# Kernel tuning notes

Hardware: AMD Instinct MI355X
Metric: run time of the kernel (lower is better)

Reference implementation:

```python
import math
import jax, jax.numpy as jnp
import numpy as np

HEADS = 16
MASKED_BIAS = -10000.0


def setup_inputs() -> dict:
    key = jax.random.key(0)
    kq, kk, kv = jax.random.split(key, 3)
    B, S, D = 4, 1024, 2048
    q = jax.random.normal(kq, (B, S, D), dtype=jnp.float32)
    k = jax.random.normal(kk, (B, S, D), dtype=jnp.float32)
    v = jax.random.normal(kv, (B, S, D), dtype=jnp.float32)
    return {"q": q, "k": k, "v": v}


def _mha(q, k, v):
    B, Sq, D = q.shape
    Sk = k.shape[-2]
    hd = D // HEADS
    # (B, H, S, hd)
    qh = q.reshape(B, Sq, HEADS, hd).transpose(0, 2, 1, 3)
    kh = k.reshape(B, Sk, HEADS, hd).transpose(0, 2, 1, 3)
    vh = v.reshape(B, Sk, HEADS, hd).transpose(0, 2, 1, 3)
    scores = jnp.einsum("bhqd,bhkd->bhqk", qh, kh) / math.sqrt(hd)
    # causal mask: query i attends to keys <= i (aligned to end of kv)
    qi = jnp.arange(Sq)[:, None] + (Sk - Sq)
    ki = jnp.arange(Sk)[None, :]
    causal = ki <= qi  # (Sq, Sk)
    scores = jnp.where(causal[None, None], scores, jnp.asarray(MASKED_BIAS, scores.dtype))
    attn = jax.nn.softmax(scores, axis=-1)
    out = jnp.einsum("bhqk,bhkd->bhqd", attn, vh)
    return out.transpose(0, 2, 1, 3).reshape(B, Sq, D)


def reference(q, k, v):
    return _mha(q, k, v)
```

## Files before the change

### kernel.cpp

```cpp
#include <hip/hip_runtime.h>
#include <hip/hip_bf16.h>


#define HEADS  16
#define HD     128
#define SEQ    1024
#define DMODEL 2048

typedef _Float16 f16;
typedef __attribute__((ext_vector_type(8))) _Float16 f16x8;
typedef __attribute__((ext_vector_type(4))) _Float16 f16x4;
typedef __attribute__((ext_vector_type(4))) float    f32x4;
typedef __attribute__((ext_vector_type(4))) unsigned int u32x4;

__device__ __forceinline__ unsigned int pkrtz(float a, float b) {
    return __builtin_bit_cast(unsigned int, __builtin_amdgcn_cvt_pkrtz(a, b));
}

__global__ __launch_bounds__(256, 2)
void fa_fwd(const float* __restrict__ Q,
            const float* __restrict__ K,
            const float* __restrict__ V,
            float* __restrict__ O)
{
    __shared__ f16 kT[64 * 128];
    __shared__ f16 vT[128 * 64];

    const int tid  = threadIdx.x;
    const int lane = tid & 63;
    const int wv   = tid >> 6;
    const int quad = lane >> 4;
    const int cl   = lane & 15;

    const int bh = blockIdx.x;
    const int qt = 15 - blockIdx.y;
    const int qb = qt * 64;
    const long long head_off = ((long long)(bh >> 4) * SEQ) * DMODEL
                             + (long long)(bh & 15) * HD;
    const float rscale = 0.08838834764831845f;

    const int krow = tid >> 4;
    const int kg   = tid & 15;
    const int kgs  = kg ^ krow;
    const int vr0  = (tid & 31) * 2;
    const int vcg  = tid >> 5;
    const int vg   = vr0 >> 3;
    const int vo   = vr0 & 7;

    f32x4 kraw[8], vraw[8];

    auto loadKV = [&](int kbase) {
        #pragma unroll
        for (int i = 0; i < 4; ++i) {
            const float* kp = K + head_off + (long long)(kbase + krow + i * 16) * DMODEL + kg * 8;
            kraw[2 * i]     = *(const f32x4*)kp;
            kraw[2 * i + 1] = *(const f32x4*)(kp + 4);
        }
        const float* vp = V + head_off + (long long)(kbase + vr0) * DMODEL + vcg * 16;
        #pragma unroll
        for (int j = 0; j < 4; ++j) {
            vraw[j]     = *(const f32x4*)(vp + 4 * j);
            vraw[4 + j] = *(const f32x4*)(vp + DMODEL + 4 * j);
        }
    };

    const int qrow = qb + wv * 16 + cl;
    f16x8 qf[4];
    {
        const float* qp = Q + head_off + (long long)qrow * DMODEL + quad * 8;
        #pragma unroll
        for (int kk = 0; kk < 4; ++kk) {
            f32x4 qa = *(const f32x4*)(qp + kk * 32);
            f32x4 qc = *(const f32x4*)(qp + kk * 32 + 4);
            union { f16x8 v; unsigned int u[4]; } qw;
            qw.u[0] = pkrtz(qa[0], qa[1]);
            qw.u[1] = pkrtz(qa[2], qa[3]);
            qw.u[2] = pkrtz(qc[0], qc[1]);
            qw.u[3] = pkrtz(qc[2], qc[3]);
            qf[kk] = qw.v;
        }
    }

    f32x4 acc[8];
    #pragma unroll
    for (int i = 0; i < 8; ++i) acc[i] = (f32x4){0.f, 0.f, 0.f, 0.f};
    float ls = 0.f;

    loadKV(0);

    #pragma unroll 1
    for (int kt = 0; kt <= qt; ++kt) {
        __syncthreads();

        #pragma unroll
        for (int i = 0; i < 4; ++i) {
            u32x4 w;
            w.x = pkrtz(kraw[2 * i][0], kraw[2 * i][1]);
            w.y = pkrtz(kraw[2 * i][2], kraw[2 * i][3]);
            w.z = pkrtz(kraw[2 * i + 1][0], kraw[2 * i + 1][1]);
            w.w = pkrtz(kraw[2 * i + 1][2], kraw[2 * i + 1][3]);
            *(u32x4*)&kT[(krow + 16 * i) * 128 + kgs * 8] = w;
        }
        #pragma unroll
        for (int j = 0; j < 16; ++j) {
            unsigned int pk = pkrtz(vraw[j >> 2][j & 3], vraw[4 + (j >> 2)][j & 3]);
            *(unsigned int*)&vT[(vcg * 16 + j) * 64 + ((vg ^ (j & 7)) * 8) + vo] = pk;
        }
        __syncthreads();

        if (kt < qt) loadKV((kt + 1) * 64);

        f32x4 sc[4];
        #pragma unroll
        for (int st = 0; st < 4; ++st) sc[st] = (f32x4){0.f, 0.f, 0.f, 0.f};
        #pragma unroll
        for (int kk = 0; kk < 4; ++kk) {
            #pragma unroll
            for (int st = 0; st < 4; ++st) {
                f16x8 kf = *(const f16x8*)&kT[(st * 16 + cl) * 128
                                              + ((kk * 4 + quad) ^ cl) * 8];
                sc[st] = __builtin_amdgcn_mfma_f32_16x16x32_f16(kf, qf[kk], sc[st], 0, 0, 0);
            }
        }

        const int kbase = kt * 64;
        f16x4 pf[4];
        if (kt == qt) {
            #pragma unroll
            for (int st = 0; st < 4; ++st) {
                float e[4];
                #pragma unroll
                for (int r = 0; r < 4; ++r) {
                    int key = kbase + st * 16 + quad * 4 + r;
                    float ex = __expf(sc[st][r] * rscale);
                    e[r] = (key <= qrow) ? ex : 0.f;
                    ls += e[r];
                }
                union { f16x4 v; unsigned int u[2]; } pw;
                pw.u[0] = pkrtz(e[0], e[1]);
                pw.u[1] = pkrtz(e[2], e[3]);
                pf[st] = pw.v;
            }
        } else {
            #pragma unroll
            for (int st = 0; st < 4; ++st) {
                float e[4];
                #pragma unroll
                for (int r = 0; r < 4; ++r) {
                    e[r] = __expf(sc[st][r] * rscale);
                    ls += e[r];
                }
                union { f16x4 v; unsigned int u[2]; } pw;
                pw.u[0] = pkrtz(e[0], e[1]);
                pw.u[1] = pkrtz(e[2], e[3]);
                pf[st] = pw.v;
            }
        }

        #pragma unroll
        for (int dt = 0; dt < 8; ++dt) {
            #pragma unroll
            for (int st = 0; st < 4; ++st) {
                f16x4 vf = *(const f16x4*)&vT[(dt * 16 + cl) * 64
                                              + ((st * 2 + (quad >> 1)) ^ (cl & 7)) * 8
                                              + (quad & 1) * 4];
                acc[dt] = __builtin_amdgcn_mfma_f32_16x16x16f16(vf, pf[st], acc[dt], 0, 0, 0);
            }
        }
    }

    float lsum = ls;
    lsum += __shfl_xor(lsum, 16, 64);
    lsum += __shfl_xor(lsum, 32, 64);
    const float rl = 1.0f / lsum;

    float* op = O + head_off + (long long)qrow * DMODEL + quad * 4;
    #pragma unroll
    for (int dt = 0; dt < 8; ++dt) {
        f32x4 o4 = acc[dt];
        o4[0] *= rl; o4[1] *= rl; o4[2] *= rl; o4[3] *= rl;
        *(f32x4*)(op + dt * 16) = o4;
    }
}

extern "C" void kernel_launch(void* const* d_in, const int* in_sizes, int n_in,
                              void* d_out, int out_size, void* d_ws, size_t ws_size,
                              hipStream_t stream) {
    const float* q = (const float*)d_in[0];
    const float* k = (const float*)d_in[1];
    const float* v = (const float*)d_in[2];
    float* o = (float*)d_out;

    dim3 grid(4 * HEADS, SEQ / 64);
    dim3 block(256);
    fa_fwd<<<grid, block, 0, stream>>>(q, k, v, o);
}
```

Before: 169.2 us.

## Process two 64-row query tiles per block to reuse each K/V tile

```diff
diff --git a/kernel.cpp b/kernel.cpp
--- a/kernel.cpp
+++ b/kernel.cpp
@@ -33,8 +33,9 @@
     const int cl   = lane & 15;
 
     const int bh = blockIdx.x;
-    const int qt = 15 - blockIdx.y;
-    const int qb = qt * 64;
+    const int yy = blockIdx.y;
+    const int qt = (yy < 4) ? (7 - yy) : (yy - 4);
+    const int qb = qt * 128;
     const long long head_off = ((long long)(bh >> 4) * SEQ) * DMODEL
                              + (long long)(bh & 15) * HD;
     const float rscale = 0.08838834764831845f;
@@ -64,10 +65,12 @@
         }
     };
 
-    const int qrow = qb + wv * 16 + cl;
-    f16x8 qf[4];
-    {
-        const float* qp = Q + head_off + (long long)qrow * DMODEL + quad * 8;
+    const int qrow0 = qb + wv * 16 + cl;
+    const int qrow1 = qrow0 + 64;
+    f16x8 qf[2][4];
+    #pragma unroll
+    for (int g = 0; g < 2; ++g) {
+        const float* qp = Q + head_off + (long long)(g ? qrow1 : qrow0) * DMODEL + quad * 8;
         #pragma unroll
         for (int kk = 0; kk < 4; ++kk) {
             f32x4 qa = *(const f32x4*)(qp + kk * 32);
@@ -77,19 +80,23 @@
             qw.u[1] = pkrtz(qa[2], qa[3]);
             qw.u[2] = pkrtz(qc[0], qc[1]);
             qw.u[3] = pkrtz(qc[2], qc[3]);
-            qf[kk] = qw.v;
-        }
-    }
-
-    f32x4 acc[8];
+            qf[g][kk] = qw.v;
+        }
+    }
+
+    f32x4 acc[8][2];
     #pragma unroll
-    for (int i = 0; i < 8; ++i) acc[i] = (f32x4){0.f, 0.f, 0.f, 0.f};
-    float ls = 0.f;
+    for (int i = 0; i < 8; ++i) {
+        acc[i][0] = (f32x4){0.f, 0.f, 0.f, 0.f};
+        acc[i][1] = (f32x4){0.f, 0.f, 0.f, 0.f};
+    }
+    float ls0 = 0.f, ls1 = 0.f;
 
     loadKV(0);
+    const int last = 2 * qt + 1;
 
     #pragma unroll 1
-    for (int kt = 0; kt <= qt; ++kt) {
+    for (int kt = 0; kt <= last; ++kt) {
         __syncthreads();
 
         #pragma unroll
@@ -108,78 +115,133 @@
         }
         __syncthreads();
 
-        if (kt < qt) loadKV((kt + 1) * 64);
-
-        f32x4 sc[4];
-        #pragma unroll
-        for (int st = 0; st < 4; ++st) sc[st] = (f32x4){0.f, 0.f, 0.f, 0.f};
-        #pragma unroll
-        for (int kk = 0; kk < 4; ++kk) {
+        if (kt < last) loadKV((kt + 1) * 64);
+
+        const int kbase = kt * 64;
+        f16x4 pf[4][2];
+
+        if (kt <= 2 * qt) {
+            f32x4 sc[4][2];
             #pragma unroll
             for (int st = 0; st < 4; ++st) {
-                f16x8 kf = *(const f16x8*)&kT[(st * 16 + cl) * 128
-                                              + ((kk * 4 + quad) ^ cl) * 8];
-                sc[st] = __builtin_amdgcn_mfma_f32_16x16x32_f16(kf, qf[kk], sc[st], 0, 0, 0);
-            }
-        }
-
-        const int kbase = kt * 64;
-        f16x4 pf[4];
-        if (kt == qt) {
+                sc[st][0] = (f32x4){0.f, 0.f, 0.f, 0.f};
+                sc[st][1] = (f32x4){0.f, 0.f, 0.f, 0.f};
+            }
+            #pragma unroll
+            for (int kk = 0; kk < 4; ++kk) {
+                #pragma unroll
+                for (int st = 0; st < 4; ++st) {
+                    f16x8 kf = *(const f16x8*)&kT[(st * 16 + cl) * 128
+                                                  + ((kk * 4 + quad) ^ cl) * 8];
+                    sc[st][0] = __builtin_amdgcn_mfma_f32_16x16x32_f16(kf, qf[0][kk], sc[st][0], 0, 0, 0);
+                    sc[st][1] = __builtin_amdgcn_mfma_f32_16x16x32_f16(kf, qf[1][kk], sc[st][1], 0, 0, 0);
+                }
+            }
+
+            if (kt == 2 * qt) {
+                #pragma unroll
+                for (int st = 0; st < 4; ++st) {
+                    float e0[4], e1[4];
+                    #pragma unroll
+                    for (int r = 0; r < 4; ++r) {
+                        const int key = kbase + st * 16 + quad * 4 + r;
+                        float ex = __expf(sc[st][0][r] * rscale);
+                        e0[r] = (key <= qrow0) ? ex : 0.f;
+                        e1[r] = __expf(sc[st][1][r] * rscale);
+                        ls0 += e0[r]; ls1 += e1[r];
+                    }
+                    union { f16x4 v; unsigned int u[2]; } p0, p1;
+                    p0.u[0] = pkrtz(e0[0], e0[1]); p0.u[1] = pkrtz(e0[2], e0[3]);
+                    p1.u[0] = pkrtz(e1[0], e1[1]); p1.u[1] = pkrtz(e1[2], e1[3]);
+                    pf[st][0] = p0.v; pf[st][1] = p1.v;
+                }
+            } else {
+                #pragma unroll
+                for (int st = 0; st < 4; ++st) {
+                    float e0[4], e1[4];
+                    #pragma unroll
+                    for (int r = 0; r < 4; ++r) {
+                        e0[r] = __expf(sc[st][0][r] * rscale);
+                        e1[r] = __expf(sc[st][1][r] * rscale);
+                        ls0 += e0[r]; ls1 += e1[r];
+                    }
+                    union { f16x4 v; unsigned int u[2]; } p0, p1;
+                    p0.u[0] = pkrtz(e0[0], e0[1]); p0.u[1] = pkrtz(e0[2], e0[3]);
+                    p1.u[0] = pkrtz(e1[0], e1[1]); p1.u[1] = pkrtz(e1[2], e1[3]);
+                    pf[st][0] = p0.v; pf[st][1] = p1.v;
+                }
+            }
+
+            #pragma unroll
+            for (int dt = 0; dt < 8; ++dt) {
+                #pragma unroll
+                for (int st = 0; st < 4; ++st) {
+                    f16x4 vf = *(const f16x4*)&vT[(dt * 16 + cl) * 64
+                                                  + ((st * 2 + (quad >> 1)) ^ (cl & 7)) * 8
+                                                  + (quad & 1) * 4];
+                    acc[dt][0] = __builtin_amdgcn_mfma_f32_16x16x16f16(vf, pf[st][0], acc[dt][0], 0, 0, 0);
+                    acc[dt][1] = __builtin_amdgcn_mfma_f32_16x16x16f16(vf, pf[st][1], acc[dt][1], 0, 0, 0);
+                }
+            }
+        } else {
+            f32x4 sc1[4];
+            #pragma unroll
+            for (int st = 0; st < 4; ++st) sc1[st] = (f32x4){0.f, 0.f, 0.f, 0.f};
+            #pragma unroll
+            for (int kk = 0; kk < 4; ++kk) {
+                #pragma unroll
+                for (int st = 0; st < 4; ++st) {
+                    f16x8 kf = *(const f16x8*)&kT[(st * 16 + cl) * 128
+                                                  + ((kk * 4 + quad) ^ cl) * 8];
+                    sc1[st] = __builtin_amdgcn_mfma_f32_16x16x32_f16(kf, qf[1][kk], sc1[st], 0, 0, 0);
+                }
+            }
             #pragma unroll
             for (int st = 0; st < 4; ++st) {
-                float e[4];
+                float e1[4];
                 #pragma unroll
                 for (int r = 0; r < 4; ++r) {
-                    int key = kbase + st * 16 + quad * 4 + r;
-                    float ex = __expf(sc[st][r] * rscale);
-                    e[r] = (key <= qrow) ? ex : 0.f;
-                    ls += e[r];
-                }
-                union { f16x4 v; unsigned int u[2]; } pw;
-                pw.u[0] = pkrtz(e[0], e[1]);
-                pw.u[1] = pkrtz(e[2], e[3]);
-                pf[st] = pw.v;
-            }
-        } else {
-            #pragma unroll
-            for (int st = 0; st < 4; ++st) {
-                float e[4];
-                #pragma unroll
-                for (int r = 0; r < 4; ++r) {
-                    e[r] = __expf(sc[st][r] * rscale);
-                    ls += e[r];
-                }
-                union { f16x4 v; unsigned int u[2]; } pw;
-                pw.u[0] = pkrtz(e[0], e[1]);
-                pw.u[1] = pkrtz(e[2], e[3]);
-                pf[st] = pw.v;
-            }
-        }
-
-        #pragma unroll
-        for (int dt = 0; dt < 8; ++dt) {
-            #pragma unroll
-            for (int st = 0; st < 4; ++st) {
-                f16x4 vf = *(const f16x4*)&vT[(dt * 16 + cl) * 64
-                                              + ((st * 2 + (quad >> 1)) ^ (cl & 7)) * 8
-                                              + (quad & 1) * 4];
-                acc[dt] = __builtin_amdgcn_mfma_f32_16x16x16f16(vf, pf[st], acc[dt], 0, 0, 0);
-            }
-        }
-    }
-
-    float lsum = ls;
-    lsum += __shfl_xor(lsum, 16, 64);
-    lsum += __shfl_xor(lsum, 32, 64);
-    const float rl = 1.0f / lsum;
-
-    float* op = O + head_off + (long long)qrow * DMODEL + quad * 4;
+                    const int key = kbase + st * 16 + quad * 4 + r;
+                    float ex = __expf(sc1[st][r] * rscale);
+                    e1[r] = (key <= qrow1) ? ex : 0.f;
+                    ls1 += e1[r];
+                }
+                union { f16x4 v; unsigned int u[2]; } p1;
+                p1.u[0] = pkrtz(e1[0], e1[1]); p1.u[1] = pkrtz(e1[2], e1[3]);
+                pf[st][1] = p1.v;
+            }
+            #pragma unroll
+            for (int dt = 0; dt < 8; ++dt) {
+                #pragma unroll
+                for (int st = 0; st < 4; ++st) {
+                    f16x4 vf = *(const f16x4*)&vT[(dt * 16 + cl) * 64
+                                                  + ((st * 2 + (quad >> 1)) ^ (cl & 7)) * 8
+                                                  + (quad & 1) * 4];
+                    acc[dt][1] = __builtin_amdgcn_mfma_f32_16x16x16f16(vf, pf[st][1], acc[dt][1], 0, 0, 0);
+                }
+            }
+        }
+    }
+
+    float l0 = ls0;
+    l0 += __shfl_xor(l0, 16, 64);
+    l0 += __shfl_xor(l0, 32, 64);
+    float l1 = ls1;
+    l1 += __shfl_xor(l1, 16, 64);
+    l1 += __shfl_xor(l1, 32, 64);
+    const float rl0 = 1.0f / l0;
+    const float rl1 = 1.0f / l1;
+
+    float* op0 = O + head_off + (long long)qrow0 * DMODEL + quad * 4;
+    float* op1 = O + head_off + (long long)qrow1 * DMODEL + quad * 4;
     #pragma unroll
     for (int dt = 0; dt < 8; ++dt) {
-        f32x4 o4 = acc[dt];
-        o4[0] *= rl; o4[1] *= rl; o4[2] *= rl; o4[3] *= rl;
-        *(f32x4*)(op + dt * 16) = o4;
+        f32x4 a = acc[dt][0];
+        a[0] *= rl0; a[1] *= rl0; a[2] *= rl0; a[3] *= rl0;
+        *(f32x4*)(op0 + dt * 16) = a;
+        f32x4 b = acc[dt][1];
+        b[0] *= rl1; b[1] *= rl1; b[2] *= rl1; b[3] *= rl1;
+        *(f32x4*)(op1 + dt * 16) = b;
     }
 }
 
@@ -191,7 +253,7 @@
     const float* v = (const float*)d_in[2];
     float* o = (float*)d_out;
 
-    dim3 grid(4 * HEADS, SEQ / 64);
+    dim3 grid(4 * HEADS, SEQ / 128);
     dim3 block(256);
     fa_fwd<<<grid, block, 0, stream>>>(q, k, v, o);
 }
```

Result: slower. 200.1 us (+18.3%).

## Split long causal query tiles across two blocks and merge partials

Applied to the files above, without the earlier changes.

```diff
diff --git a/kernel.cpp b/kernel.cpp
--- a/kernel.cpp
+++ b/kernel.cpp
@@ -13,15 +13,19 @@
 typedef __attribute__((ext_vector_type(4))) float    f32x4;
 typedef __attribute__((ext_vector_type(4))) unsigned int u32x4;
 
+#define WS_PAIR_FLOATS 16512
+#define WS_NEEDED (512ull * WS_PAIR_FLOATS * 4ull)
+
 __device__ __forceinline__ unsigned int pkrtz(float a, float b) {
     return __builtin_bit_cast(unsigned int, __builtin_amdgcn_cvt_pkrtz(a, b));
 }
 
-__global__ __launch_bounds__(256, 2)
+__global__ __launch_bounds__(256, 4)
 void fa_fwd(const float* __restrict__ Q,
             const float* __restrict__ K,
             const float* __restrict__ V,
-            float* __restrict__ O)
+            float* __restrict__ O,
+            float* __restrict__ WS)
 {
     __shared__ f16 kT[64 * 128];
     __shared__ f16 vT[128 * 64];
@@ -33,8 +37,21 @@
     const int cl   = lane & 15;
 
     const int bh = blockIdx.x;
-    const int qt = 15 - blockIdx.y;
+    const int yy = blockIdx.y;
+
+    int qt, kt0, kt1, split, nsplit;
+    if (gridDim.y == 16) {
+        qt = 15 - yy; kt0 = 0; kt1 = qt + 1; split = 0; nsplit = 1;
+    } else if (yy < 16) {
+        qt = 15 - (yy >> 1); split = yy & 1; nsplit = 2;
+        const int h = (qt + 1) >> 1;
+        kt0 = split ? h : 0;
+        kt1 = split ? qt + 1 : h;
+    } else {
+        qt = 23 - yy; kt0 = 0; kt1 = qt + 1; split = 0; nsplit = 1;
+    }
     const int qb = qt * 64;
+
     const long long head_off = ((long long)(bh >> 4) * SEQ) * DMODEL
                              + (long long)(bh & 15) * HD;
     const float rscale = 0.08838834764831845f;
@@ -86,10 +103,10 @@
     for (int i = 0; i < 8; ++i) acc[i] = (f32x4){0.f, 0.f, 0.f, 0.f};
     float ls = 0.f;
 
-    loadKV(0);
+    loadKV(kt0 * 64);
 
     #pragma unroll 1
-    for (int kt = 0; kt <= qt; ++kt) {
+    for (int kt = kt0; kt < kt1; ++kt) {
         __syncthreads();
 
         #pragma unroll
@@ -108,7 +125,7 @@
         }
         __syncthreads();
 
-        if (kt < qt) loadKV((kt + 1) * 64);
+        if (kt < kt1 - 1) loadKV((kt + 1) * 64);
 
         f32x4 sc[4];
         #pragma unroll
@@ -172,15 +189,62 @@
     float lsum = ls;
     lsum += __shfl_xor(lsum, 16, 64);
     lsum += __shfl_xor(lsum, 32, 64);
-    const float rl = 1.0f / lsum;
-
-    float* op = O + head_off + (long long)qrow * DMODEL + quad * 4;
+
+    if (nsplit == 1) {
+        const float rl = 1.0f / lsum;
+        float* op = O + head_off + (long long)qrow * DMODEL + quad * 4;
+        #pragma unroll
+        for (int dt = 0; dt < 8; ++dt) {
+            f32x4 o4 = acc[dt];
+            o4[0] *= rl; o4[1] *= rl; o4[2] *= rl; o4[3] *= rl;
+            *(f32x4*)(op + dt * 16) = o4;
+        }
+        return;
+    }
+
+    const int pairIdx = bh * 8 + (qt - 8);
+    float* base  = WS + (long long)pairIdx * WS_PAIR_FLOATS;
+    float* myNum = base + split * 8192;
+    float* myDen = base + 16384 + split * 64;
+    const int rloc = wv * 16 + cl;
+
+    float* np = myNum + rloc * 128 + quad * 4;
     #pragma unroll
     for (int dt = 0; dt < 8; ++dt) {
-        f32x4 o4 = acc[dt];
-        o4[0] *= rl; o4[1] *= rl; o4[2] *= rl; o4[3] *= rl;
-        *(f32x4*)(op + dt * 16) = o4;
-    }
+        *(f32x4*)(np + dt * 16) = acc[dt];
+    }
+    if (quad == 0) myDen[rloc] = lsum;
+}
+
+__global__ __launch_bounds__(256, 8)
+void fa_merge(const float* __restrict__ WS, float* __restrict__ O)
+{
+    const int bid  = blockIdx.x;
+    const int pair = bid >> 3;
+    const int sub  = bid & 7;
+    const int bh   = pair >> 3;
+    const int qt   = (pair & 7) + 8;
+    const long long head_off = ((long long)(bh >> 4) * SEQ) * DMODEL
+                             + (long long)(bh & 15) * HD;
+    const float* base = WS + (long long)pair * WS_PAIR_FLOATS;
+
+    const int i   = sub * 256 + threadIdx.x;
+    const int row = i >> 5;
+    const int c4  = i & 31;
+
+    const float d0 = base[16384 + row];
+    const float d1 = base[16448 + row];
+    const float rl = 1.0f / (d0 + d1);
+
+    const f32x4 n0 = *(const f32x4*)(base + row * 128 + c4 * 4);
+    const f32x4 n1 = *(const f32x4*)(base + 8192 + row * 128 + c4 * 4);
+    f32x4 o;
+    o[0] = (n0[0] + n1[0]) * rl;
+    o[1] = (n0[1] + n1[1]) * rl;
+    o[2] = (n0[2] + n1[2]) * rl;
+    o[3] = (n0[3] + n1[3]) * rl;
+
+    *(f32x4*)(O + head_off + (long long)(qt * 64 + row) * DMODEL + c4 * 4) = o;
 }
 
 extern "C" void kernel_launch(void* const* d_in, const int* in_sizes, int n_in,
@@ -191,7 +255,13 @@
     const float* v = (const float*)d_in[2];
     float* o = (float*)d_out;
 
-    dim3 grid(4 * HEADS, SEQ / 64);
-    dim3 block(256);
-    fa_fwd<<<grid, block, 0, stream>>>(q, k, v, o);
-}
+    const bool do_split = (d_ws != nullptr) && (ws_size >= WS_NEEDED);
+    if (do_split) {
+        dim3 grid(4 * HEADS, 24);
+        fa_fwd<<<grid, dim3(256), 0, stream>>>(q, k, v, o, (float*)d_ws);
+        fa_merge<<<dim3(4096), dim3(256), 0, stream>>>((const float*)d_ws, o);
+    } else {
+        dim3 grid(4 * HEADS, 16);
+        fa_fwd<<<grid, dim3(256), 0, stream>>>(q, k, v, o, (float*)d_ws);
+    }
+}
```

Result: slower. 301.7 us (+78.4%).

## Shrink attention tiles to 32 queries and 32 keys with 128-thread blocks

Applied to the files above, without the earlier changes.

```diff
diff --git a/kernel.cpp b/kernel.cpp
--- a/kernel.cpp
+++ b/kernel.cpp
@@ -17,14 +17,14 @@
     return __builtin_bit_cast(unsigned int, __builtin_amdgcn_cvt_pkrtz(a, b));
 }
 
-__global__ __launch_bounds__(256, 2)
+__global__ __launch_bounds__(128, 2)
 void fa_fwd(const float* __restrict__ Q,
             const float* __restrict__ K,
             const float* __restrict__ V,
             float* __restrict__ O)
 {
-    __shared__ f16 kT[64 * 128];
-    __shared__ f16 vT[128 * 64];
+    __shared__ f16 kT[32 * 128];
+    __shared__ f16 vT[128 * 32];
 
     const int tid  = threadIdx.x;
     const int lane = tid & 63;
@@ -33,26 +33,25 @@
     const int cl   = lane & 15;
 
     const int bh = blockIdx.x;
-    const int qt = 15 - blockIdx.y;
-    const int qb = qt * 64;
+    const int qt = 31 - blockIdx.y;
+    const int qb = qt * 32;
     const long long head_off = ((long long)(bh >> 4) * SEQ) * DMODEL
                              + (long long)(bh & 15) * HD;
     const float rscale = 0.08838834764831845f;
 
     const int krow = tid >> 4;
     const int kg   = tid & 15;
-    const int kgs  = kg ^ krow;
-    const int vr0  = (tid & 31) * 2;
-    const int vcg  = tid >> 5;
-    const int vg   = vr0 >> 3;
-    const int vo   = vr0 & 7;
+    const int vr0  = (tid & 15) * 2;
+    const int vcg  = tid >> 4;
+    const int vslot = vr0 >> 2;
+    const int vsub  = (vr0 & 3) >> 1;
 
     f32x4 kraw[8], vraw[8];
 
     auto loadKV = [&](int kbase) {
         #pragma unroll
         for (int i = 0; i < 4; ++i) {
-            const float* kp = K + head_off + (long long)(kbase + krow + i * 16) * DMODEL + kg * 8;
+            const float* kp = K + head_off + (long long)(kbase + krow + 8 * i) * DMODEL + kg * 8;
             kraw[2 * i]     = *(const f32x4*)kp;
             kraw[2 * i + 1] = *(const f32x4*)(kp + 4);
         }
@@ -94,77 +93,86 @@
 
         #pragma unroll
         for (int i = 0; i < 4; ++i) {
+            const int row = krow + 8 * i;
             u32x4 w;
             w.x = pkrtz(kraw[2 * i][0], kraw[2 * i][1]);
             w.y = pkrtz(kraw[2 * i][2], kraw[2 * i][3]);
             w.z = pkrtz(kraw[2 * i + 1][0], kraw[2 * i + 1][1]);
             w.w = pkrtz(kraw[2 * i + 1][2], kraw[2 * i + 1][3]);
-            *(u32x4*)&kT[(krow + 16 * i) * 128 + kgs * 8] = w;
+            *(u32x4*)&kT[row * 128 + (kg ^ (row & 15)) * 8] = w;
         }
         #pragma unroll
         for (int j = 0; j < 16; ++j) {
+            const int d = vcg * 16 + j;
             unsigned int pk = pkrtz(vraw[j >> 2][j & 3], vraw[4 + (j >> 2)][j & 3]);
-            *(unsigned int*)&vT[(vcg * 16 + j) * 64 + ((vg ^ (j & 7)) * 8) + vo] = pk;
+            ((unsigned int*)vT)[d * 16 + (vslot ^ (d & 7)) * 2 + vsub] = pk;
         }
         __syncthreads();
 
-        if (kt < qt) loadKV((kt + 1) * 64);
-
-        f32x4 sc[4];
-        #pragma unroll
-        for (int st = 0; st < 4; ++st) sc[st] = (f32x4){0.f, 0.f, 0.f, 0.f};
+        if (kt < qt) loadKV((kt + 1) * 32);
+
+        const bool diag  = (kt == qt);
+        const bool dead1 = diag && (wv == 0);
+
+        f32x4 sc[2];
+        sc[0] = (f32x4){0.f, 0.f, 0.f, 0.f};
+        sc[1] = (f32x4){0.f, 0.f, 0.f, 0.f};
         #pragma unroll
         for (int kk = 0; kk < 4; ++kk) {
+            f16x8 kf0 = *(const f16x8*)&kT[(cl) * 128 + ((kk * 4 + quad) ^ cl) * 8];
+            sc[0] = __builtin_amdgcn_mfma_f32_16x16x32_f16(kf0, qf[kk], sc[0], 0, 0, 0);
+            if (!dead1) {
+                f16x8 kf1 = *(const f16x8*)&kT[(16 + cl) * 128 + ((kk * 4 + quad) ^ cl) * 8];
+                sc[1] = __builtin_amdgcn_mfma_f32_16x16x32_f16(kf1, qf[kk], sc[1], 0, 0, 0);
+            }
+        }
+
+        const int kbase = kt * 32;
+        f16x4 pf[2];
+        {
+            float e[4];
             #pragma unroll
-            for (int st = 0; st < 4; ++st) {
-                f16x8 kf = *(const f16x8*)&kT[(st * 16 + cl) * 128
-                                              + ((kk * 4 + quad) ^ cl) * 8];
-                sc[st] = __builtin_amdgcn_mfma_f32_16x16x32_f16(kf, qf[kk], sc[st], 0, 0, 0);
-            }
-        }
-
-        const int kbase = kt * 64;
-        f16x4 pf[4];
-        if (kt == qt) {
+            for (int r = 0; r < 4; ++r) {
+                float ex = __expf(sc[0][r] * rscale);
+                if (diag && wv == 0) {
+                    int key = kbase + quad * 4 + r;
+                    ex = (key <= qrow) ? ex : 0.f;
+                }
+                e[r] = ex;
+                ls += e[r];
+            }
+            union { f16x4 v; unsigned int u[2]; } pw;
+            pw.u[0] = pkrtz(e[0], e[1]);
+            pw.u[1] = pkrtz(e[2], e[3]);
+            pf[0] = pw.v;
+        }
+        if (!dead1) {
+            float e[4];
             #pragma unroll
-            for (int st = 0; st < 4; ++st) {
-                float e[4];
-                #pragma unroll
-                for (int r = 0; r < 4; ++r) {
-                    int key = kbase + st * 16 + quad * 4 + r;
-                    float ex = __expf(sc[st][r] * rscale);
-                    e[r] = (key <= qrow) ? ex : 0.f;
-                    ls += e[r];
+            for (int r = 0; r < 4; ++r) {
+                float ex = __expf(sc[1][r] * rscale);
+                if (diag && wv == 1) {
+                    int key = kbase + 16 + quad * 4 + r;
+                    ex = (key <= qrow) ? ex : 0.f;
                 }
-                union { f16x4 v; unsigned int u[2]; } pw;
-                pw.u[0] = pkrtz(e[0], e[1]);
-                pw.u[1] = pkrtz(e[2], e[3]);
-                pf[st] = pw.v;
-            }
-        } else {
-            #pragma unroll
-            for (int st = 0; st < 4; ++st) {
-                float e[4];
-                #pragma unroll
-                for (int r = 0; r < 4; ++r) {
-                    e[r] = __expf(sc[st][r] * rscale);
-                    ls += e[r];
-                }
-                union { f16x4 v; unsigned int u[2]; } pw;
-                pw.u[0] = pkrtz(e[0], e[1]);
-                pw.u[1] = pkrtz(e[2], e[3]);
-                pf[st] = pw.v;
-            }
+                e[r] = ex;
+                ls += e[r];
+            }
+            union { f16x4 v; unsigned int u[2]; } pw;
+            pw.u[0] = pkrtz(e[0], e[1]);
+            pw.u[1] = pkrtz(e[2], e[3]);
+            pf[1] = pw.v;
         }
 
         #pragma unroll
         for (int dt = 0; dt < 8; ++dt) {
-            #pragma unroll
-            for (int st = 0; st < 4; ++st) {
-                f16x4 vf = *(const f16x4*)&vT[(dt * 16 + cl) * 64
-                                              + ((st * 2 + (quad >> 1)) ^ (cl & 7)) * 8
-                                              + (quad & 1) * 4];
-                acc[dt] = __builtin_amdgcn_mfma_f32_16x16x16f16(vf, pf[st], acc[dt], 0, 0, 0);
+            f16x4 vf0 = *(const f16x4*)&vT[(dt * 16 + cl) * 32
+                                           + ((quad) ^ (cl & 7)) * 4];
+            acc[dt] = __builtin_amdgcn_mfma_f32_16x16x16f16(vf0, pf[0], acc[dt], 0, 0, 0);
+            if (!dead1) {
+                f16x4 vf1 = *(const f16x4*)&vT[(dt * 16 + cl) * 32
+                                               + ((4 + quad) ^ (cl & 7)) * 4];
+                acc[dt] = __builtin_amdgcn_mfma_f32_16x16x16f16(vf1, pf[1], acc[dt], 0, 0, 0);
             }
         }
     }
@@ -191,7 +199,7 @@
     const float* v = (const float*)d_in[2];
     float* o = (float*)d_out;
 
-    dim3 grid(4 * HEADS, SEQ / 64);
-    dim3 block(256);
+    dim3 grid(4 * HEADS, SEQ / 32);
+    dim3 block(128);
     fa_fwd<<<grid, block, 0, stream>>>(q, k, v, o);
 }
```

Measured after the change: 205.1 us. 1.21x slower.
